# Kernel tuning notes

Hardware: AMD Instinct MI355X
Metric: run time of the kernel (lower is better)

## Reference

```python
import jax, jax.numpy as jnp
import numpy as np
from jax import lax

HID = 256
BATCH = 256
INPUT_LEN = 512
N_SAMPLES = 16
HORIZON = 64


def _lstm_cell(x, h, c, Wih, Whh, b):
    # x: [B, in], h/c: [B, H]; PyTorch gate order i, f, g, o; b = b_ih + b_hh
    gates = x @ Wih.T + h @ Whh.T + b  # [B, 4H]
    i, f, g, o = jnp.split(gates, 4, axis=-1)
    c_new = jax.nn.sigmoid(f) * c + jax.nn.sigmoid(i) * jnp.tanh(g)
    h_new = jax.nn.sigmoid(o) * jnp.tanh(c_new)
    return h_new, c_new


def setup_inputs() -> dict:
    key = jax.random.key(0)
    ks = jax.random.split(key, 20)
    s = 1.0 / np.sqrt(HID)  # PyTorch LSTM init scale
    def u(k, shape):
        return jax.random.uniform(k, shape, jnp.float32, -s, s)
    inp = {
        "x": jax.random.normal(ks[0], (BATCH, INPUT_LEN), jnp.float32),
        "enc_Wih0": u(ks[1], (4 * HID, 1)),
        "enc_Whh0": u(ks[2], (4 * HID, HID)),
        "enc_b0": u(ks[3], (4 * HID,)),
        "enc_Wih1": u(ks[4], (4 * HID, HID)),
        "enc_Whh1": u(ks[5], (4 * HID, HID)),
        "enc_b1": u(ks[6], (4 * HID,)),
        "dec_Wih0": u(ks[7], (4 * HID, 1)),
        "dec_Whh0": u(ks[8], (4 * HID, HID)),
        "dec_b0": u(ks[9], (4 * HID,)),
        "dec_Wih1": u(ks[10], (4 * HID, HID)),
        "dec_Whh1": u(ks[11], (4 * HID, HID)),
        "dec_b1": u(ks[12], (4 * HID,)),
        "out_W": u(ks[13], (1, HID)),
        "out_b": u(ks[14], (1,)),
        # torch.rand(batch,1,1) per sample -> stacked over n_samples
        "dec_init": jax.random.uniform(ks[15], (N_SAMPLES, BATCH, 1), jnp.float32),
        "horizon": HORIZON,
    }
    return inp


def reference(x, enc_Wih0, enc_Whh0, enc_b0, enc_Wih1, enc_Whh1, enc_b1,
              dec_Wih0, dec_Whh0, dec_b0, dec_Wih1, dec_Whh1, dec_b1,
              out_W, out_b, dec_init, horizon):
    B, T = x.shape
    S = dec_init.shape[0]
    H = enc_Whh0.shape[1]

    # ---- encoder: 2-layer LSTM over input sequence ----
    xs = x.T[:, :, None]  # [T, B, 1]
    zero = jnp.zeros((B, H), x.dtype)

    def enc_step(carry, xt):
        h0, c0, h1, c1 = carry
        h0, c0 = _lstm_cell(xt, h0, c0, enc_Wih0, enc_Whh0, enc_b0)
        h1, c1 = _lstm_cell(h0, h1, c1, enc_Wih1, enc_Whh1, enc_b1)
        return (h0, c0, h1, c1), None

    (h0, c0, h1, c1), _ = lax.scan(enc_step, (zero, zero, zero, zero), xs)

    # ---- decoder: batch the independent n_samples together ----
    def rep(t):  # [B,H] -> [S*B,H]
        return jnp.broadcast_to(t, (S, B, H)).reshape(S * B, H)

    inp0 = dec_init.reshape(S * B, 1)

    def dec_step(carry, _):
        inp, h0, c0, h1, c1 = carry
        h0, c0 = _lstm_cell(inp, h0, c0, dec_Wih0, dec_Whh0, dec_b0)
        h1, c1 = _lstm_cell(h0, h1, c1, dec_Wih1, dec_Whh1, dec_b1)
        pred = h1 @ out_W.T + out_b  # [S*B, 1]
        return (pred, h0, c0, h1, c1), pred

    carry0 = (inp0, rep(h0), rep(c0), rep(h1), rep(c1))
    _, preds = lax.scan(dec_step, carry0, None, length=horizon)
    # preds: [T, S*B, 1] -> [B, S, T]
    return preds[:, :, 0].reshape(horizon, S, B).transpose(2, 1, 0)
```

## Files before the change

kernel.cpp:

```cpp
#include <hip/hip_runtime.h>
#include <stdint.h>


typedef short short8v __attribute__((ext_vector_type(8)));
typedef float float4v __attribute__((ext_vector_type(4)));
typedef unsigned long long u64;
#define MFMA(a,b,c) __builtin_amdgcn_mfma_f32_16x16x32_bf16((a),(b),(c),0,0,0)

#define HIDN 256
#define TLEN 512
#define HPE  ((size_t)256 * HIDN)
#define HPD  ((size_t)4096 * HIDN)

__device__ __forceinline__ unsigned short f2b(float f) {
    unsigned int u = __float_as_uint(f);
    unsigned int r = ((u >> 16) & 1u) + 0x7FFFu;
    return (unsigned short)((u + r) >> 16);
}
__device__ __forceinline__ float sigf(float x) { return 1.0f / (1.0f + __expf(-x)); }
__device__ __forceinline__ float tanhf2(float x) { return 1.0f - 2.0f / (1.0f + __expf(2.0f * x)); }

__device__ __forceinline__ void hpair_store(unsigned short* buf, int row, int hid,
                                            float h, int lane) {
    unsigned int mine = f2b(h);
    unsigned int part = (unsigned int)__shfl_xor((int)mine, 1);
    if (!(lane & 1)) {
        __hip_atomic_store((unsigned int*)&buf[(size_t)row * HIDN + hid],
                           mine | (part << 16),
                           __ATOMIC_RELAXED, __HIP_MEMORY_SCOPE_AGENT);
    }
}

__device__ __forceinline__ void bar_sync(unsigned int* fl, int slot, unsigned int target,
                                         int lane, int tid, int& dead) {
    __syncthreads();
    if (tid == 0)
        __hip_atomic_store(&fl[slot], target, __ATOMIC_RELAXED, __HIP_MEMORY_SCOPE_AGENT);
    if (!dead) {
        int guard = 0;
        for (;;) {
            unsigned int v = 0xFFFFFFFFu;
            if (lane < 16)
                v = __hip_atomic_load(&fl[lane], __ATOMIC_RELAXED, __HIP_MEMORY_SCOPE_AGENT);
            if (__ballot(v >= target) == ~0ull) break;
            if (++guard > (1 << 20)) { dead = 1; break; }
        }
    }
    __builtin_amdgcn_fence(__ATOMIC_ACQUIRE, "workgroup");
}

__global__ __launch_bounds__(256) void pack_kernel(
    const float* __restrict__ Whh0, const float* __restrict__ Wih1,
    const float* __restrict__ Whh1, unsigned short* __restrict__ pk)
{
    int gid = blockIdx.x * 256 + threadIdx.x;
    int lane = gid & 63;
    int kc = (gid >> 6) & 7;
    int n  = (gid >> 9) & 63;
    int mat = gid >> 15;
    const float* W = (mat == 0) ? Whh0 : ((mat == 1) ? Wih1 : Whh1);
    const float* p = W + (size_t)(n * 16 + (lane & 15)) * HIDN
                       + (kc << 5) + ((lane >> 4) << 3);
    short8v v;
#pragma unroll
    for (int i = 0; i < 8; ++i) v[i] = (short)f2b(p[i]);
    *(short8v*)&pk[(size_t)gid << 3] = v;
}

__global__ __launch_bounds__(256, 1) void enc_kernel(
    const float* __restrict__ x,
    const float* __restrict__ Wih0, const float* __restrict__ Whh0, const float* __restrict__ b0,
    const float* __restrict__ Wih1, const float* __restrict__ Whh1, const float* __restrict__ b1,
    unsigned short* __restrict__ h0e, unsigned short* __restrict__ h1e,
    unsigned short* __restrict__ finh0, unsigned short* __restrict__ finh1,
    float* __restrict__ finc0, float* __restrict__ finc1,
    unsigned int* __restrict__ flags)
{
    const int tid = threadIdx.x, lane = tid & 63, wv = tid >> 6;
    const int bt = blockIdx.x & 15, hs = blockIdx.x >> 4;
    const int row0 = bt << 4, hidb = hs << 4;
    const int l15 = lane & 15, q = lane >> 4, q8 = q << 3;

    __shared__ float gt[12][16][17];
    __shared__ float xt[16][TLEN + 1];
    __shared__ unsigned short hst0[16][264], hst1[16][264];

    for (int idx = tid; idx < 16 * TLEN; idx += 256) {
        int r = idx >> 9, c = idx & 511;
        xt[r][c] = x[(size_t)(row0 + r) * TLEN + c];
    }

    short8v wf[3][8];
    {
        const float* Ws[3] = {Whh0, Wih1, Whh1};
#pragma unroll
        for (int j = 0; j < 3; ++j) {
            int p = wv * 3 + j;
            int mat = p >> 2, g = p & 3;
            const float* rp = Ws[mat] + (size_t)((g << 8) + hidb + l15) * HIDN + q8;
#pragma unroll
            for (int kc = 0; kc < 8; ++kc) {
                short8v v;
#pragma unroll
                for (int i = 0; i < 8; ++i) v[i] = (short)f2b(rp[(kc << 5) + i]);
                wf[j][kc] = v;
            }
        }
    }

    const int erow = tid >> 4, ehid = tid & 15;
    const int grow = row0 + erow, ghid = hidb + ehid;
    float wx[4], bb0v[4], bb1v[4];
#pragma unroll
    for (int g = 0; g < 4; ++g) {
        wx[g]   = Wih0[(g << 8) + ghid];
        bb0v[g] = b0[(g << 8) + ghid];
        bb1v[g] = b1[(g << 8) + ghid];
    }
    float c0 = 0.f, c1 = 0.f;
    unsigned int* fl = flags + (bt << 4);
    int dead = 0;
    const bool useH0 = (wv <= 2), useH1 = (wv >= 2);
    __syncthreads();

    for (int s = 1; s <= 513; ++s) {
        const unsigned short* hr0 = h0e + (size_t)((s - 1) & 1) * HPE;
        const unsigned short* hr1 = h1e + (size_t)((s - 1) & 1) * HPE;
        unsigned short* hw0 = h0e + (size_t)(s & 1) * HPE;
        unsigned short* hw1 = h1e + (size_t)(s & 1) * HPE;

        if (s >= 2) {
#pragma unroll
            for (int k = 0; k < 4; ++k) {
                int oo = tid + (k << 8);
                int r = oo >> 6, cu = oo & 63;
                u64 v = __hip_atomic_load((const u64*)&hr0[(size_t)(row0 + r) * HIDN + (cu << 2)],
                                          __ATOMIC_RELAXED, __HIP_MEMORY_SCOPE_AGENT);
                *(u64*)&hst0[r][cu << 2] = v;
            }
        }
        if (s >= 3) {
#pragma unroll
            for (int k = 0; k < 4; ++k) {
                int oo = tid + (k << 8);
                int r = oo >> 6, cu = oo & 63;
                u64 v = __hip_atomic_load((const u64*)&hr1[(size_t)(row0 + r) * HIDN + (cu << 2)],
                                          __ATOMIC_RELAXED, __HIP_MEMORY_SCOPE_AGENT);
                *(u64*)&hst1[r][cu << 2] = v;
            }
        }
        __syncthreads();

        float4v acc[3] = {{0,0,0,0},{0,0,0,0},{0,0,0,0}};
        short8v a0f[8], a1f[8];
        if (useH0 && s >= 2) {
#pragma unroll
            for (int kc = 0; kc < 8; ++kc) a0f[kc] = *(const short8v*)&hst0[l15][(kc << 5) + q8];
        }
        if (useH1 && s >= 3) {
#pragma unroll
            for (int kc = 0; kc < 8; ++kc) a1f[kc] = *(const short8v*)&hst1[l15][(kc << 5) + q8];
        }
#pragma unroll
        for (int j = 0; j < 3; ++j) {
            int p = wv * 3 + j;
            int mat = p >> 2;
            bool active = (mat == 0) ? (s >= 2 && s <= 512)
                        : (mat == 1) ? (s >= 2)
                                     : (s >= 3);
            if (active) {
                if (mat == 2) {
#pragma unroll
                    for (int kc = 0; kc < 8; ++kc) acc[j] = MFMA(a1f[kc], wf[j][kc], acc[j]);
                } else {
#pragma unroll
                    for (int kc = 0; kc < 8; ++kc) acc[j] = MFMA(a0f[kc], wf[j][kc], acc[j]);
                }
            }
        }
#pragma unroll
        for (int j = 0; j < 3; ++j) {
            int p = wv * 3 + j;
#pragma unroll
            for (int r = 0; r < 4; ++r) gt[p][(q << 2) + r][l15] = acc[j][r];
        }
        __syncthreads();

        if (s <= 512) {
            float xv = xt[erow][s - 1];
            float gi = gt[0][erow][ehid] + wx[0] * xv + bb0v[0];
            float gf = gt[1][erow][ehid] + wx[1] * xv + bb0v[1];
            float gg = gt[2][erow][ehid] + wx[2] * xv + bb0v[2];
            float go = gt[3][erow][ehid] + wx[3] * xv + bb0v[3];
            c0 = sigf(gf) * c0 + sigf(gi) * tanhf2(gg);
            float h0n = sigf(go) * tanhf2(c0);
            hpair_store(hw0, grow, ghid, h0n, lane);
            if (s == 512) {
                finh0[(size_t)grow * HIDN + ghid] = f2b(h0n);
                finc0[(size_t)grow * HIDN + ghid] = c0;
            }
        }
        if (s >= 2) {
            float gi = gt[4][erow][ehid] + gt[8][erow][ehid]  + bb1v[0];
            float gf = gt[5][erow][ehid] + gt[9][erow][ehid]  + bb1v[1];
            float gg = gt[6][erow][ehid] + gt[10][erow][ehid] + bb1v[2];
            float go = gt[7][erow][ehid] + gt[11][erow][ehid] + bb1v[3];
            c1 = sigf(gf) * c1 + sigf(gi) * tanhf2(gg);
            float h1n = sigf(go) * tanhf2(c1);
            hpair_store(hw1, grow, ghid, h1n, lane);
            if (s == 513) {
                finh1[(size_t)grow * HIDN + ghid] = f2b(h1n);
                finc1[(size_t)grow * HIDN + ghid] = c1;
            }
        }
        bar_sync(fl, hs, (unsigned int)s, lane, tid, dead);
    }
}

__global__ __launch_bounds__(256, 1) void decA_kernel(
    const unsigned short* __restrict__ pk,
    const float* __restrict__ Wih0, const float* __restrict__ b0,
    const float* __restrict__ outb, const float* __restrict__ dinit,
    const unsigned short* __restrict__ finh0, const float* __restrict__ finc0,
    const unsigned short* __restrict__ h0in, unsigned short* __restrict__ h0out,
    float* __restrict__ c0buf, const float* __restrict__ predprev,
    float* __restrict__ out, int t)
{
    extern __shared__ unsigned short wlds[];
    const int tid = threadIdx.x, lane = tid & 63, wv = tid >> 6;
    const int rg = blockIdx.x >> 3, hsl = blockIdx.x & 7;
    const int row0 = rg << 7, hidb = hsl << 5;
    const int l15 = lane & 15, q = lane >> 4, q8 = q << 3;

#pragma unroll
    for (int k = 0; k < 16; ++k) {
        int sl = tid + (k << 8);
        int ln = sl & 63, kc = (sl >> 6) & 7, nf = sl >> 9;
        int n = ((nf >> 1) << 4) + (hsl << 1) + (nf & 1);
        *(short8v*)&wlds[sl << 3] =
            *(const short8v*)&pk[((size_t)((n << 3) + kc) << 9) + (ln << 3)];
    }
    short8v af[2][8];
#pragma unroll
    for (int m = 0; m < 2; ++m) {
        int row = row0 + (wv << 5) + (m << 4) + l15;
        const unsigned short* p = (t == 0) ? finh0 + (size_t)(row & 255) * HIDN + q8
                                           : h0in + (size_t)row * HIDN + q8;
#pragma unroll
        for (int kc = 0; kc < 8; ++kc) af[m][kc] = *(const short8v*)&p[kc << 5];
    }
    __syncthreads();

    float4v acc[2][8];
#pragma unroll
    for (int m = 0; m < 2; ++m)
#pragma unroll
        for (int nf = 0; nf < 8; ++nf) acc[m][nf] = (float4v){0, 0, 0, 0};
#pragma unroll
    for (int kc = 0; kc < 8; ++kc)
#pragma unroll
        for (int nf = 0; nf < 8; ++nf) {
            short8v bf = *(const short8v*)&wlds[(size_t)(((((nf << 3) + kc) << 6) + lane) << 3)];
            acc[0][nf] = MFMA(af[0][kc], bf, acc[0][nf]);
            acc[1][nf] = MFMA(af[1][kc], bf, acc[1][nf]);
        }

    const float outb_v = outb[0];
    float wx2[2][4], bb2[2][4];
#pragma unroll
    for (int u = 0; u < 2; ++u) {
        int hid = hidb + (u << 4) + l15;
#pragma unroll
        for (int g = 0; g < 4; ++g) {
            wx2[u][g] = Wih0[(g << 8) + hid];
            bb2[u][g] = b0[(g << 8) + hid];
        }
    }
#pragma unroll
    for (int m = 0; m < 2; ++m)
#pragma unroll
        for (int u = 0; u < 2; ++u) {
            int hid = hidb + (u << 4) + l15;
#pragma unroll
            for (int r = 0; r < 4; ++r) {
                int row = row0 + (wv << 5) + (m << 4) + (q << 2) + r;
                float inp = (t == 0) ? dinit[row] : (predprev[row] + outb_v);
                float cold = (t == 0) ? finc0[(size_t)(row & 255) * HIDN + hid]
                                      : c0buf[(size_t)row * HIDN + hid];
                float gi = acc[m][0 + u][r] + wx2[u][0] * inp + bb2[u][0];
                float gf = acc[m][2 + u][r] + wx2[u][1] * inp + bb2[u][1];
                float gg = acc[m][4 + u][r] + wx2[u][2] * inp + bb2[u][2];
                float go = acc[m][6 + u][r] + wx2[u][3] * inp + bb2[u][3];
                float cn = sigf(gf) * cold + sigf(gi) * tanhf2(gg);
                c0buf[(size_t)row * HIDN + hid] = cn;
                float h0n = sigf(go) * tanhf2(cn);
                unsigned int mine = f2b(h0n);
                unsigned int part = (unsigned int)__shfl_xor((int)mine, 1);
                if (!(lane & 1))
                    *(unsigned int*)&h0out[(size_t)row * HIDN + hid] = mine | (part << 16);
            }
        }
    if (hsl == 0 && t > 0 && tid < 128) {
        int row = row0 + tid;
        out[(size_t)(((row & 255) << 4) + (row >> 8)) * 64 + (t - 1)] = predprev[row] + outb_v;
    }
}

__global__ __launch_bounds__(256, 1) void decB_kernel(
    const unsigned short* __restrict__ pk,
    const float* __restrict__ b1, const float* __restrict__ outW,
    const unsigned short* __restrict__ finh1, const float* __restrict__ finc1,
    const unsigned short* __restrict__ h0cur, const unsigned short* __restrict__ h1in,
    unsigned short* __restrict__ h1out, float* __restrict__ c1buf,
    float* __restrict__ predcur, int t)
{
    extern __shared__ unsigned short wlds[];
    const int tid = threadIdx.x, lane = tid & 63, wv = tid >> 6;
    const int rg = blockIdx.x >> 3, hsl = blockIdx.x & 7;
    const int row0 = rg << 7, hidb = hsl << 5;
    const int l15 = lane & 15, q = lane >> 4, q8 = q << 3;

#pragma unroll
    for (int k = 0; k < 32; ++k) {
        int sl = tid + (k << 8);
        int ln = sl & 63, kc = (sl >> 6) & 7, nf = (sl >> 9) & 7, mt = sl >> 12;
        int n = ((mt + 1) << 6) + ((nf >> 1) << 4) + (hsl << 1) + (nf & 1);
        *(short8v*)&wlds[sl << 3] =
            *(const short8v*)&pk[((size_t)((n << 3) + kc) << 9) + (ln << 3)];
    }
    short8v a0[2][8], a1[2][8];
#pragma unroll
    for (int m = 0; m < 2; ++m) {
        int row = row0 + (wv << 5) + (m << 4) + l15;
        const unsigned short* p0 = h0cur + (size_t)row * HIDN + q8;
        const unsigned short* p1 = (t == 0) ? finh1 + (size_t)(row & 255) * HIDN + q8
                                            : h1in + (size_t)row * HIDN + q8;
#pragma unroll
        for (int kc = 0; kc < 8; ++kc) {
            a0[m][kc] = *(const short8v*)&p0[kc << 5];
            a1[m][kc] = *(const short8v*)&p1[kc << 5];
        }
    }
    __syncthreads();

    float4v acc[2][8];
#pragma unroll
    for (int m = 0; m < 2; ++m)
#pragma unroll
        for (int nf = 0; nf < 8; ++nf) acc[m][nf] = (float4v){0, 0, 0, 0};
#pragma unroll
    for (int kc = 0; kc < 8; ++kc)
#pragma unroll
        for (int nf = 0; nf < 8; ++nf) {
            short8v bf = *(const short8v*)&wlds[(size_t)(((((nf << 3) + kc) << 6) + lane) << 3)];
            acc[0][nf] = MFMA(a0[0][kc], bf, acc[0][nf]);
            acc[1][nf] = MFMA(a0[1][kc], bf, acc[1][nf]);
        }
#pragma unroll
    for (int kc = 0; kc < 8; ++kc)
#pragma unroll
        for (int nf = 0; nf < 8; ++nf) {
            short8v bf = *(const short8v*)&wlds[(size_t)((((32768 >> 3) + (((nf << 3) + kc) << 6) + lane) << 3))];
            acc[0][nf] = MFMA(a1[0][kc], bf, acc[0][nf]);
            acc[1][nf] = MFMA(a1[1][kc], bf, acc[1][nf]);
        }

    float ow2[2], bb2[2][4];
#pragma unroll
    for (int u = 0; u < 2; ++u) {
        int hid = hidb + (u << 4) + l15;
        ow2[u] = outW[hid];
#pragma unroll
        for (int g = 0; g < 4; ++g) bb2[u][g] = b1[(g << 8) + hid];
    }
    float pp[2][4] = {{0,0,0,0},{0,0,0,0}};
#pragma unroll
    for (int m = 0; m < 2; ++m)
#pragma unroll
        for (int u = 0; u < 2; ++u) {
            int hid = hidb + (u << 4) + l15;
#pragma unroll
            for (int r = 0; r < 4; ++r) {
                int row = row0 + (wv << 5) + (m << 4) + (q << 2) + r;
                float cold = (t == 0) ? finc1[(size_t)(row & 255) * HIDN + hid]
                                      : c1buf[(size_t)row * HIDN + hid];
                float gi = acc[m][0 + u][r] + bb2[u][0];
                float gf = acc[m][2 + u][r] + bb2[u][1];
                float gg = acc[m][4 + u][r] + bb2[u][2];
                float go = acc[m][6 + u][r] + bb2[u][3];
                float cn = sigf(gf) * cold + sigf(gi) * tanhf2(gg);
                c1buf[(size_t)row * HIDN + hid] = cn;
                float h1n = sigf(go) * tanhf2(cn);
                pp[m][r] += h1n * ow2[u];
                unsigned int mine = f2b(h1n);
                unsigned int part = (unsigned int)__shfl_xor((int)mine, 1);
                if (!(lane & 1))
                    *(unsigned int*)&h1out[(size_t)row * HIDN + hid] = mine | (part << 16);
            }
        }
#pragma unroll
    for (int off = 1; off < 16; off <<= 1)
#pragma unroll
        for (int m = 0; m < 2; ++m)
#pragma unroll
            for (int r = 0; r < 4; ++r) pp[m][r] += __shfl_xor(pp[m][r], off);
    if (l15 == 0) {
#pragma unroll
        for (int m = 0; m < 2; ++m)
#pragma unroll
            for (int r = 0; r < 4; ++r) {
                int row = row0 + (wv << 5) + (m << 4) + (q << 2) + r;
                atomicAdd(&predcur[row], pp[m][r]);
            }
    }
}

__global__ __launch_bounds__(256) void decC_kernel(const float* __restrict__ pred63,
                                                   const float* __restrict__ outb,
                                                   float* __restrict__ out) {
    int row = blockIdx.x * 256 + threadIdx.x;
    out[(size_t)(((row & 255) << 4) + (row >> 8)) * 64 + 63] = pred63[row] + outb[0];
}

extern "C" void kernel_launch(void* const* d_in, const int* in_sizes, int n_in,
                              void* d_out, int out_size, void* d_ws, size_t ws_size,
                              hipStream_t stream) {
    (void)in_sizes; (void)n_in; (void)out_size; (void)ws_size;
    const float* x     = (const float*)d_in[0];
    const float* eWih0 = (const float*)d_in[1];
    const float* eWhh0 = (const float*)d_in[2];
    const float* eb0   = (const float*)d_in[3];
    const float* eWih1 = (const float*)d_in[4];
    const float* eWhh1 = (const float*)d_in[5];
    const float* eb1   = (const float*)d_in[6];
    const float* dWih0 = (const float*)d_in[7];
    const float* dWhh0 = (const float*)d_in[8];
    const float* db0   = (const float*)d_in[9];
    const float* dWih1 = (const float*)d_in[10];
    const float* dWhh1 = (const float*)d_in[11];
    const float* db1   = (const float*)d_in[12];
    const float* outW  = (const float*)d_in[13];
    const float* outb  = (const float*)d_in[14];
    const float* dinit = (const float*)d_in[15];

    char* ws = (char*)d_ws;
    unsigned short* h0e   = (unsigned short*)(ws);
    unsigned short* h1e   = (unsigned short*)(ws + 262144);
    unsigned short* finh0 = (unsigned short*)(ws + 524288);
    unsigned short* finh1 = (unsigned short*)(ws + 655360);
    float* finc0          = (float*)(ws + 786432);
    float* finc1          = (float*)(ws + 1048576);
    unsigned int* fle     = (unsigned int*)(ws + 1310720);
    unsigned short* pk    = (unsigned short*)(ws + 1311744);
    unsigned short* h0d   = (unsigned short*)(ws + 2884608);
    unsigned short* h1d   = (unsigned short*)(ws + 7078912);
    float* c0buf          = (float*)(ws + 11273216);
    float* c1buf          = (float*)(ws + 15467520);
    float* predraw        = (float*)(ws + 19661824);

    hipMemsetAsync(fle, 0, 1024, stream);
    hipMemsetAsync(predraw, 0, 64 * 4096 * 4, stream);
    hipFuncSetAttribute((const void*)decA_kernel,
                        hipFuncAttributeMaxDynamicSharedMemorySize, 65536);
    hipFuncSetAttribute((const void*)decB_kernel,
                        hipFuncAttributeMaxDynamicSharedMemorySize, 131072);

    pack_kernel<<<384, 256, 0, stream>>>(dWhh0, dWih1, dWhh1, pk);
    enc_kernel<<<256, 256, 0, stream>>>(x, eWih0, eWhh0, eb0, eWih1, eWhh1, eb1,
                                        h0e, h1e, finh0, finh1, finc0, finc1, fle);
    for (int t = 0; t < 64; ++t) {
        const unsigned short* h0in = h0d + (size_t)((t + 1) & 1) * HPD;
        unsigned short* h0o        = h0d + (size_t)(t & 1) * HPD;
        const unsigned short* h1in = h1d + (size_t)((t + 1) & 1) * HPD;
        unsigned short* h1o        = h1d + (size_t)(t & 1) * HPD;
        const float* pprev = predraw + (size_t)(t > 0 ? (t - 1) : 0) * 4096;
        decA_kernel<<<256, 256, 65536, stream>>>(pk, dWih0, db0, outb, dinit,
                                                 finh0, finc0, h0in, h0o, c0buf,
                                                 pprev, (float*)d_out, t);
        decB_kernel<<<256, 256, 131072, stream>>>(pk, db1, outW, finh1, finc1,
                                                  h0o, h1in, h1o, c1buf,
                                                  predraw + (size_t)t * 4096, t);
    }
    decC_kernel<<<16, 256, 0, stream>>>(predraw + (size_t)63 * 4096, outb, (float*)d_out);
}
```

Before: 4.594 ms.

## Fuse decoder steps into one persistent kernel with inter-block flag barriers

```diff
diff --git a/kernel.cpp b/kernel.cpp
--- a/kernel.cpp
+++ b/kernel.cpp
@@ -29,6 +29,13 @@
                            mine | (part << 16),
                            __ATOMIC_RELAXED, __HIP_MEMORY_SCOPE_AGENT);
     }
+}
+
+__device__ __forceinline__ short8v ldA16(const unsigned short* p) {
+    union { u64 d[2]; short8v v; } w;
+    w.d[0] = __hip_atomic_load((const u64*)p,     __ATOMIC_RELAXED, __HIP_MEMORY_SCOPE_AGENT);
+    w.d[1] = __hip_atomic_load((const u64*)p + 1, __ATOMIC_RELAXED, __HIP_MEMORY_SCOPE_AGENT);
+    return w.v;
 }
 
 __device__ __forceinline__ void bar_sync(unsigned int* fl, int slot, unsigned int target,
@@ -49,6 +56,24 @@
     __builtin_amdgcn_fence(__ATOMIC_ACQUIRE, "workgroup");
 }
 
+__device__ __forceinline__ void bar8_sync(unsigned int* fl, int slot, unsigned int target,
+                                          int lane, int tid, int& dead) {
+    __syncthreads();
+    if (tid == 0)
+        __hip_atomic_store(&fl[slot], target, __ATOMIC_RELAXED, __HIP_MEMORY_SCOPE_AGENT);
+    if (!dead) {
+        int guard = 0;
+        for (;;) {
+            unsigned int v = 0xFFFFFFFFu;
+            if (lane < 8)
+                v = __hip_atomic_load(&fl[lane], __ATOMIC_RELAXED, __HIP_MEMORY_SCOPE_AGENT);
+            if (__ballot(v >= target) == ~0ull) break;
+            if (++guard > (1 << 20)) { dead = 1; break; }
+        }
+    }
+    __builtin_amdgcn_fence(__ATOMIC_ACQUIRE, "workgroup");
+}
+
 __global__ __launch_bounds__(256) void pack_kernel(
     const float* __restrict__ Whh0, const float* __restrict__ Wih1,
     const float* __restrict__ Whh1, unsigned short* __restrict__ pk)
@@ -217,106 +242,20 @@
     }
 }
 
-__global__ __launch_bounds__(256, 1) void decA_kernel(
+__global__ __launch_bounds__(256, 1) void dec_kernel(
     const unsigned short* __restrict__ pk,
     const float* __restrict__ Wih0, const float* __restrict__ b0,
+    const float* __restrict__ b1, const float* __restrict__ outW,
     const float* __restrict__ outb, const float* __restrict__ dinit,
     const unsigned short* __restrict__ finh0, const float* __restrict__ finc0,
-    const unsigned short* __restrict__ h0in, unsigned short* __restrict__ h0out,
-    float* __restrict__ c0buf, const float* __restrict__ predprev,
-    float* __restrict__ out, int t)
+    const unsigned short* __restrict__ finh1, const float* __restrict__ finc1,
+    unsigned short* __restrict__ h0d, unsigned short* __restrict__ h1d,
+    float* __restrict__ predbuf, unsigned int* __restrict__ flags,
+    float* __restrict__ out)
 {
     extern __shared__ unsigned short wlds[];
     const int tid = threadIdx.x, lane = tid & 63, wv = tid >> 6;
-    const int rg = blockIdx.x >> 3, hsl = blockIdx.x & 7;
-    const int row0 = rg << 7, hidb = hsl << 5;
-    const int l15 = lane & 15, q = lane >> 4, q8 = q << 3;
-
-#pragma unroll
-    for (int k = 0; k < 16; ++k) {
-        int sl = tid + (k << 8);
-        int ln = sl & 63, kc = (sl >> 6) & 7, nf = sl >> 9;
-        int n = ((nf >> 1) << 4) + (hsl << 1) + (nf & 1);
-        *(short8v*)&wlds[sl << 3] =
-            *(const short8v*)&pk[((size_t)((n << 3) + kc) << 9) + (ln << 3)];
-    }
-    short8v af[2][8];
-#pragma unroll
-    for (int m = 0; m < 2; ++m) {
-        int row = row0 + (wv << 5) + (m << 4) + l15;
-        const unsigned short* p = (t == 0) ? finh0 + (size_t)(row & 255) * HIDN + q8
-                                           : h0in + (size_t)row * HIDN + q8;
-#pragma unroll
-        for (int kc = 0; kc < 8; ++kc) af[m][kc] = *(const short8v*)&p[kc << 5];
-    }
-    __syncthreads();
-
-    float4v acc[2][8];
-#pragma unroll
-    for (int m = 0; m < 2; ++m)
-#pragma unroll
-        for (int nf = 0; nf < 8; ++nf) acc[m][nf] = (float4v){0, 0, 0, 0};
-#pragma unroll
-    for (int kc = 0; kc < 8; ++kc)
-#pragma unroll
-        for (int nf = 0; nf < 8; ++nf) {
-            short8v bf = *(const short8v*)&wlds[(size_t)(((((nf << 3) + kc) << 6) + lane) << 3)];
-            acc[0][nf] = MFMA(af[0][kc], bf, acc[0][nf]);
-            acc[1][nf] = MFMA(af[1][kc], bf, acc[1][nf]);
-        }
-
-    const float outb_v = outb[0];
-    float wx2[2][4], bb2[2][4];
-#pragma unroll
-    for (int u = 0; u < 2; ++u) {
-        int hid = hidb + (u << 4) + l15;
-#pragma unroll
-        for (int g = 0; g < 4; ++g) {
-            wx2[u][g] = Wih0[(g << 8) + hid];
-            bb2[u][g] = b0[(g << 8) + hid];
-        }
-    }
-#pragma unroll
-    for (int m = 0; m < 2; ++m)
-#pragma unroll
-        for (int u = 0; u < 2; ++u) {
-            int hid = hidb + (u << 4) + l15;
-#pragma unroll
-            for (int r = 0; r < 4; ++r) {
-                int row = row0 + (wv << 5) + (m << 4) + (q << 2) + r;
-                float inp = (t == 0) ? dinit[row] : (predprev[row] + outb_v);
-                float cold = (t == 0) ? finc0[(size_t)(row & 255) * HIDN + hid]
-                                      : c0buf[(size_t)row * HIDN + hid];
-                float gi = acc[m][0 + u][r] + wx2[u][0] * inp + bb2[u][0];
-                float gf = acc[m][2 + u][r] + wx2[u][1] * inp + bb2[u][1];
-                float gg = acc[m][4 + u][r] + wx2[u][2] * inp + bb2[u][2];
-                float go = acc[m][6 + u][r] + wx2[u][3] * inp + bb2[u][3];
-                float cn = sigf(gf) * cold + sigf(gi) * tanhf2(gg);
-                c0buf[(size_t)row * HIDN + hid] = cn;
-                float h0n = sigf(go) * tanhf2(cn);
-                unsigned int mine = f2b(h0n);
-                unsigned int part = (unsigned int)__shfl_xor((int)mine, 1);
-                if (!(lane & 1))
-                    *(unsigned int*)&h0out[(size_t)row * HIDN + hid] = mine | (part << 16);
-            }
-        }
-    if (hsl == 0 && t > 0 && tid < 128) {
-        int row = row0 + tid;
-        out[(size_t)(((row & 255) << 4) + (row >> 8)) * 64 + (t - 1)] = predprev[row] + outb_v;
-    }
-}
-
-__global__ __launch_bounds__(256, 1) void decB_kernel(
-    const unsigned short* __restrict__ pk,
-    const float* __restrict__ b1, const float* __restrict__ outW,
-    const unsigned short* __restrict__ finh1, const float* __restrict__ finc1,
-    const unsigned short* __restrict__ h0cur, const unsigned short* __restrict__ h1in,
-    unsigned short* __restrict__ h1out, float* __restrict__ c1buf,
-    float* __restrict__ predcur, int t)
-{
-    extern __shared__ unsigned short wlds[];
-    const int tid = threadIdx.x, lane = tid & 63, wv = tid >> 6;
-    const int rg = blockIdx.x >> 3, hsl = blockIdx.x & 7;
+    const int rg = blockIdx.x & 31, hsl = blockIdx.x >> 5;
     const int row0 = rg << 7, hidb = hsl << 5;
     const int l15 = lane & 15, q = lane >> 4, q8 = q << 3;
 
@@ -328,52 +267,21 @@
         *(short8v*)&wlds[sl << 3] =
             *(const short8v*)&pk[((size_t)((n << 3) + kc) << 9) + (ln << 3)];
     }
-    short8v a0[2][8], a1[2][8];
-#pragma unroll
-    for (int m = 0; m < 2; ++m) {
-        int row = row0 + (wv << 5) + (m << 4) + l15;
-        const unsigned short* p0 = h0cur + (size_t)row * HIDN + q8;
-        const unsigned short* p1 = (t == 0) ? finh1 + (size_t)(row & 255) * HIDN + q8
-                                            : h1in + (size_t)row * HIDN + q8;
-#pragma unroll
-        for (int kc = 0; kc < 8; ++kc) {
-            a0[m][kc] = *(const short8v*)&p0[kc << 5];
-            a1[m][kc] = *(const short8v*)&p1[kc << 5];
-        }
-    }
-    __syncthreads();
-
-    float4v acc[2][8];
-#pragma unroll
-    for (int m = 0; m < 2; ++m)
-#pragma unroll
-        for (int nf = 0; nf < 8; ++nf) acc[m][nf] = (float4v){0, 0, 0, 0};
-#pragma unroll
-    for (int kc = 0; kc < 8; ++kc)
-#pragma unroll
-        for (int nf = 0; nf < 8; ++nf) {
-            short8v bf = *(const short8v*)&wlds[(size_t)(((((nf << 3) + kc) << 6) + lane) << 3)];
-            acc[0][nf] = MFMA(a0[0][kc], bf, acc[0][nf]);
-            acc[1][nf] = MFMA(a0[1][kc], bf, acc[1][nf]);
-        }
-#pragma unroll
-    for (int kc = 0; kc < 8; ++kc)
-#pragma unroll
-        for (int nf = 0; nf < 8; ++nf) {
-            short8v bf = *(const short8v*)&wlds[(size_t)((((32768 >> 3) + (((nf << 3) + kc) << 6) + lane) << 3))];
-            acc[0][nf] = MFMA(a1[0][kc], bf, acc[0][nf]);
-            acc[1][nf] = MFMA(a1[1][kc], bf, acc[1][nf]);
-        }
-
-    float ow2[2], bb2[2][4];
+
+    const float outb_v = outb[0];
+    float wx2[2][4], bb0v[2][4], bb1v[2][4], ow2[2];
 #pragma unroll
     for (int u = 0; u < 2; ++u) {
         int hid = hidb + (u << 4) + l15;
         ow2[u] = outW[hid];
 #pragma unroll
-        for (int g = 0; g < 4; ++g) bb2[u][g] = b1[(g << 8) + hid];
-    }
-    float pp[2][4] = {{0,0,0,0},{0,0,0,0}};
+        for (int g = 0; g < 4; ++g) {
+            wx2[u][g]  = Wih0[(g << 8) + hid];
+            bb0v[u][g] = b0[(g << 8) + hid];
+            bb1v[u][g] = b1[(g << 8) + hid];
+        }
+    }
+    float c0r[2][2][4], c1r[2][2][4];
 #pragma unroll
     for (int m = 0; m < 2; ++m)
 #pragma unroll
@@ -382,44 +290,157 @@
 #pragma unroll
             for (int r = 0; r < 4; ++r) {
                 int row = row0 + (wv << 5) + (m << 4) + (q << 2) + r;
-                float cold = (t == 0) ? finc1[(size_t)(row & 255) * HIDN + hid]
-                                      : c1buf[(size_t)row * HIDN + hid];
-                float gi = acc[m][0 + u][r] + bb2[u][0];
-                float gf = acc[m][2 + u][r] + bb2[u][1];
-                float gg = acc[m][4 + u][r] + bb2[u][2];
-                float go = acc[m][6 + u][r] + bb2[u][3];
-                float cn = sigf(gf) * cold + sigf(gi) * tanhf2(gg);
-                c1buf[(size_t)row * HIDN + hid] = cn;
-                float h1n = sigf(go) * tanhf2(cn);
-                pp[m][r] += h1n * ow2[u];
-                unsigned int mine = f2b(h1n);
-                unsigned int part = (unsigned int)__shfl_xor((int)mine, 1);
-                if (!(lane & 1))
-                    *(unsigned int*)&h1out[(size_t)row * HIDN + hid] = mine | (part << 16);
-            }
-        }
-#pragma unroll
-    for (int off = 1; off < 16; off <<= 1)
-#pragma unroll
-        for (int m = 0; m < 2; ++m)
-#pragma unroll
-            for (int r = 0; r < 4; ++r) pp[m][r] += __shfl_xor(pp[m][r], off);
-    if (l15 == 0) {
+                c0r[m][u][r] = finc0[(size_t)(row & 255) * HIDN + hid];
+                c1r[m][u][r] = finc1[(size_t)(row & 255) * HIDN + hid];
+            }
+        }
+    unsigned int* fl = flags + (rg << 4);
+    int dead = 0;
+    __syncthreads();
+
+    for (int t = 0; t < 64; ++t) {
+        const unsigned short* h0prev = (t == 0) ? finh0 : h0d + (size_t)((t + 1) & 1) * HPD;
+        const unsigned short* h1prev = (t == 0) ? finh1 : h1d + (size_t)((t + 1) & 1) * HPD;
+        unsigned short* h0w = h0d + (size_t)(t & 1) * HPD;
+        unsigned short* h1w = h1d + (size_t)(t & 1) * HPD;
+        const int rmask = (t == 0) ? 255 : 0x7FFFFFFF;
+
+        short8v af0[2][8], af1[2][8];
+#pragma unroll
+        for (int m = 0; m < 2; ++m) {
+            int row = (row0 + (wv << 5) + (m << 4) + l15) & rmask;
+            const unsigned short* p0 = h0prev + (size_t)row * HIDN + q8;
+            const unsigned short* p1 = h1prev + (size_t)row * HIDN + q8;
+#pragma unroll
+            for (int kc = 0; kc < 8; ++kc) {
+                af0[m][kc] = ldA16(p0 + (kc << 5));
+                af1[m][kc] = ldA16(p1 + (kc << 5));
+            }
+        }
+        float inp[2][4];
 #pragma unroll
         for (int m = 0; m < 2; ++m)
 #pragma unroll
             for (int r = 0; r < 4; ++r) {
                 int row = row0 + (wv << 5) + (m << 4) + (q << 2) + r;
-                atomicAdd(&predcur[row], pp[m][r]);
-            }
-    }
-}
-
-__global__ __launch_bounds__(256) void decC_kernel(const float* __restrict__ pred63,
-                                                   const float* __restrict__ outb,
-                                                   float* __restrict__ out) {
-    int row = blockIdx.x * 256 + threadIdx.x;
-    out[(size_t)(((row & 255) << 4) + (row >> 8)) * 64 + 63] = pred63[row] + outb[0];
+                inp[m][r] = (t == 0) ? dinit[row]
+                    : __hip_atomic_load(&predbuf[(size_t)(t - 1) * 4096 + row],
+                                        __ATOMIC_RELAXED, __HIP_MEMORY_SCOPE_AGENT) + outb_v;
+            }
+        if (hsl == 0 && t > 0 && tid < 128) {
+            int row = row0 + tid;
+            float v = __hip_atomic_load(&predbuf[(size_t)(t - 1) * 4096 + row],
+                                        __ATOMIC_RELAXED, __HIP_MEMORY_SCOPE_AGENT) + outb_v;
+            out[(size_t)(((row & 255) << 4) + (row >> 8)) * 64 + (t - 1)] = v;
+        }
+
+        float4v acc0[2][8];
+#pragma unroll
+        for (int m = 0; m < 2; ++m)
+#pragma unroll
+            for (int nf = 0; nf < 8; ++nf) acc0[m][nf] = (float4v){0, 0, 0, 0};
+#pragma unroll
+        for (int kc = 0; kc < 8; ++kc)
+#pragma unroll
+            for (int nf = 0; nf < 8; ++nf) {
+                int n = ((nf >> 1) << 4) + (hsl << 1) + (nf & 1);
+                short8v bf = *(const short8v*)&pk[((size_t)((n << 3) + kc) << 9) + (lane << 3)];
+                acc0[0][nf] = MFMA(af0[0][kc], bf, acc0[0][nf]);
+                acc0[1][nf] = MFMA(af0[1][kc], bf, acc0[1][nf]);
+            }
+        float4v acc1[2][8];
+#pragma unroll
+        for (int m = 0; m < 2; ++m)
+#pragma unroll
+            for (int nf = 0; nf < 8; ++nf) acc1[m][nf] = (float4v){0, 0, 0, 0};
+#pragma unroll
+        for (int kc = 0; kc < 8; ++kc)
+#pragma unroll
+            for (int nf = 0; nf < 8; ++nf) {
+                short8v bf = *(const short8v*)&wlds[(size_t)((((8 + nf) << 3) + kc) << 6 | lane) << 3];
+                acc1[0][nf] = MFMA(af1[0][kc], bf, acc1[0][nf]);
+                acc1[1][nf] = MFMA(af1[1][kc], bf, acc1[1][nf]);
+            }
+#pragma unroll
+        for (int m = 0; m < 2; ++m)
+#pragma unroll
+            for (int u = 0; u < 2; ++u) {
+                int hid = hidb + (u << 4) + l15;
+#pragma unroll
+                for (int r = 0; r < 4; ++r) {
+                    int row = row0 + (wv << 5) + (m << 4) + (q << 2) + r;
+                    float gi = acc0[m][0 + u][r] + wx2[u][0] * inp[m][r] + bb0v[u][0];
+                    float gf = acc0[m][2 + u][r] + wx2[u][1] * inp[m][r] + bb0v[u][1];
+                    float gg = acc0[m][4 + u][r] + wx2[u][2] * inp[m][r] + bb0v[u][2];
+                    float go = acc0[m][6 + u][r] + wx2[u][3] * inp[m][r] + bb0v[u][3];
+                    float cn = sigf(gf) * c0r[m][u][r] + sigf(gi) * tanhf2(gg);
+                    c0r[m][u][r] = cn;
+                    float h0n = sigf(go) * tanhf2(cn);
+                    hpair_store(h0w, row, hid, h0n, lane);
+                }
+            }
+        bar8_sync(fl, hsl, (unsigned int)(2 * t + 1), lane, tid, dead);
+
+        short8v af0n[2][8];
+#pragma unroll
+        for (int m = 0; m < 2; ++m) {
+            int row = row0 + (wv << 5) + (m << 4) + l15;
+            const unsigned short* p0 = h0w + (size_t)row * HIDN + q8;
+#pragma unroll
+            for (int kc = 0; kc < 8; ++kc) af0n[m][kc] = ldA16(p0 + (kc << 5));
+        }
+#pragma unroll
+        for (int kc = 0; kc < 8; ++kc)
+#pragma unroll
+            for (int nf = 0; nf < 8; ++nf) {
+                short8v bf = *(const short8v*)&wlds[(size_t)(((nf << 3) + kc) << 6 | lane) << 3];
+                acc1[0][nf] = MFMA(af0n[0][kc], bf, acc1[0][nf]);
+                acc1[1][nf] = MFMA(af0n[1][kc], bf, acc1[1][nf]);
+            }
+        float pp[2][4] = {{0,0,0,0},{0,0,0,0}};
+#pragma unroll
+        for (int m = 0; m < 2; ++m)
+#pragma unroll
+            for (int u = 0; u < 2; ++u) {
+                int hid = hidb + (u << 4) + l15;
+#pragma unroll
+                for (int r = 0; r < 4; ++r) {
+                    int row = row0 + (wv << 5) + (m << 4) + (q << 2) + r;
+                    float gi = acc1[m][0 + u][r] + bb1v[u][0];
+                    float gf = acc1[m][2 + u][r] + bb1v[u][1];
+                    float gg = acc1[m][4 + u][r] + bb1v[u][2];
+                    float go = acc1[m][6 + u][r] + bb1v[u][3];
+                    float cn = sigf(gf) * c1r[m][u][r] + sigf(gi) * tanhf2(gg);
+                    c1r[m][u][r] = cn;
+                    float h1n = sigf(go) * tanhf2(cn);
+                    pp[m][r] += h1n * ow2[u];
+                    hpair_store(h1w, row, hid, h1n, lane);
+                }
+            }
+#pragma unroll
+        for (int off = 1; off < 16; off <<= 1)
+#pragma unroll
+            for (int m = 0; m < 2; ++m)
+#pragma unroll
+                for (int r = 0; r < 4; ++r) pp[m][r] += __shfl_xor(pp[m][r], off);
+        if (l15 == 0) {
+#pragma unroll
+            for (int m = 0; m < 2; ++m)
+#pragma unroll
+                for (int r = 0; r < 4; ++r) {
+                    int row = row0 + (wv << 5) + (m << 4) + (q << 2) + r;
+                    atomicAdd(&predbuf[(size_t)t * 4096 + row], pp[m][r]);
+                }
+        }
+        bar8_sync(fl, hsl, (unsigned int)(2 * t + 2), lane, tid, dead);
+    }
+
+    if (hsl == 0 && tid < 128) {
+        int row = row0 + tid;
+        float v = __hip_atomic_load(&predbuf[(size_t)63 * 4096 + row],
+                                    __ATOMIC_RELAXED, __HIP_MEMORY_SCOPE_AGENT) + outb_v;
+        out[(size_t)(((row & 255) << 4) + (row >> 8)) * 64 + 63] = v;
+    }
 }
 
 extern "C" void kernel_launch(void* const* d_in, const int* in_sizes, int n_in,
@@ -454,32 +475,19 @@
     unsigned short* pk    = (unsigned short*)(ws + 1311744);
     unsigned short* h0d   = (unsigned short*)(ws + 2884608);
     unsigned short* h1d   = (unsigned short*)(ws + 7078912);
-    float* c0buf          = (float*)(ws + 11273216);
-    float* c1buf          = (float*)(ws + 15467520);
+    unsigned int* fld     = (unsigned int*)(ws + 11273216);
     float* predraw        = (float*)(ws + 19661824);
 
     hipMemsetAsync(fle, 0, 1024, stream);
+    hipMemsetAsync(fld, 0, 2048, stream);
     hipMemsetAsync(predraw, 0, 64 * 4096 * 4, stream);
-    hipFuncSetAttribute((const void*)decA_kernel,
-                        hipFuncAttributeMaxDynamicSharedMemorySize, 65536);
-    hipFuncSetAttribute((const void*)decB_kernel,
+    hipFuncSetAttribute((const void*)dec_kernel,
                         hipFuncAttributeMaxDynamicSharedMemorySize, 131072);
 
     pack_kernel<<<384, 256, 0, stream>>>(dWhh0, dWih1, dWhh1, pk);
     enc_kernel<<<256, 256, 0, stream>>>(x, eWih0, eWhh0, eb0, eWih1, eWhh1, eb1,
                                         h0e, h1e, finh0, finh1, finc0, finc1, fle);
-    for (int t = 0; t < 64; ++t) {
-        const unsigned short* h0in = h0d + (size_t)((t + 1) & 1) * HPD;
-        unsigned short* h0o        = h0d + (size_t)(t & 1) * HPD;
-        const unsigned short* h1in = h1d + (size_t)((t + 1) & 1) * HPD;
-        unsigned short* h1o        = h1d + (size_t)(t & 1) * HPD;
-        const float* pprev = predraw + (size_t)(t > 0 ? (t - 1) : 0) * 4096;
-        decA_kernel<<<256, 256, 65536, stream>>>(pk, dWih0, db0, outb, dinit,
-                                                 finh0, finc0, h0in, h0o, c0buf,
-                                                 pprev, (float*)d_out, t);
-        decB_kernel<<<256, 256, 131072, stream>>>(pk, db1, outW, finh1, finc1,
-                                                  h0o, h1in, h1o, c1buf,
-                                                  predraw + (size_t)t * 4096, t);
-    }
-    decC_kernel<<<16, 256, 0, stream>>>(predraw + (size_t)63 * 4096, outb, (float*)d_out);
-}
+    dec_kernel<<<256, 256, 131072, stream>>>(pk, dWih0, db0, db1, outW, outb, dinit,
+                                             finh0, finc0, finh1, finc1,
+                                             h0d, h1d, predraw, fld, (float*)d_out);
+}
```

Measured after the change: 4.272 ms. -7.0%, faster.
